# Kernel tuning notes

Measured on AMD Instinct MI355X. Metric: run time of the kernel, lower is better.

The kernel has to match this reference:

```python
import jax, jax.numpy as jnp
import numpy as np

B, S, D, H, F = 2, 4096, 768, 12, 3072
DK = D // H
EPS = 1e-5


def _layernorm(x, alpha, gamma):
    # Faithful to the custom Layernormalization: torch.std (unbiased, ddof=1),
    # (x - mean) / (std + eps), scalar alpha/gamma.
    m = jnp.mean(x, axis=-1, keepdims=True)
    s = jnp.std(x, axis=-1, ddof=1, keepdims=True)
    return alpha * ((x - m) / (s + EPS)) + gamma


def setup_inputs() -> dict:
    key = jax.random.key(0)
    ks = jax.random.split(key, 12)
    sc = 0.02
    inp = {
        "x": jax.random.normal(ks[0], (B, S, D), jnp.float32),
        # attention projections, stored as [in, out]
        "wq": jax.random.normal(ks[1], (D, D), jnp.float32) * sc,
        "bq": jnp.zeros((D,), jnp.float32),
        "wk": jax.random.normal(ks[2], (D, D), jnp.float32) * sc,
        "bk": jnp.zeros((D,), jnp.float32),
        "wv": jax.random.normal(ks[3], (D, D), jnp.float32) * sc,
        "bv": jnp.zeros((D,), jnp.float32),
        "wo": jax.random.normal(ks[4], (D, D), jnp.float32) * sc,
        "bo": jnp.zeros((D,), jnp.float32),
        # feedforward
        "w1": jax.random.normal(ks[5], (D, F), jnp.float32) * sc,
        "b1": jnp.zeros((F,), jnp.float32),
        "w2": jax.random.normal(ks[6], (F, D), jnp.float32) * sc,
        "b2": jnp.zeros((D,), jnp.float32),
        # two residual LayerNorms, scalar params (alpha=1, gamma=0 at init)
        "a1": jnp.ones((1,), jnp.float32),
        "g1": jnp.zeros((1,), jnp.float32),
        "a2": jnp.ones((1,), jnp.float32),
        "g2": jnp.zeros((1,), jnp.float32),
    }
    return inp


def reference(x, wq, bq, wk, bk, wv, bv, wo, bo, w1, b1, w2, b2, a1, g1, a2, g2):
    # --- self attention sublayer ---
    q = (x @ wq + bq).reshape(B, S, H, DK).transpose(0, 2, 1, 3)  # [B,H,S,dk]
    k = (x @ wk + bk).reshape(B, S, H, DK).transpose(0, 2, 1, 3)
    v = (x @ wv + bv).reshape(B, S, H, DK).transpose(0, 2, 1, 3)
    scores = jnp.einsum("bhqd,bhkd->bhqk", q, k) / np.sqrt(DK).astype(np.float32)
    attn = jax.nn.softmax(scores, axis=-1)  # dropout is identity (p=0 / eval)
    ctx = jnp.einsum("bhqk,bhkd->bhqd", attn, v)  # [B,H,S,dk]
    ctx = ctx.transpose(0, 2, 1, 3).reshape(B, S, D)
    attn_out = ctx @ wo + bo
    x = _layernorm(x + attn_out, a1, g1)
    # --- feedforward sublayer ---
    ff = jax.nn.relu(x @ w1 + b1) @ w2 + b2
    x = _layernorm(x + ff, a2, g2)
    return x
```

## Files before the change

### kernel.cpp

```cpp
#include <hip/hip_runtime.h>
#include <hip/hip_bf16.h>
#include <cstdint>
#include <cstddef>

typedef unsigned short u16;
typedef __attribute__((ext_vector_type(8))) __bf16 bf16x8;
typedef __attribute__((ext_vector_type(4))) float f32x4;

#define AS1 __attribute__((address_space(1)))
#define AS3 __attribute__((address_space(3)))

__device__ __forceinline__ u16 f2bf(float f) {
    union { float f; uint32_t u; } v; v.f = f;
    uint32_t r = (v.u + 0x7FFFu + ((v.u >> 16) & 1u)) >> 16;
    return (u16)r;
}

__device__ __forceinline__ float bf2f(u16 b) {
    union { uint32_t u; float f; } v; v.u = ((uint32_t)b) << 16;
    return v.f;
}

__device__ __forceinline__ uint32_t cvtpk_bf2(float lo, float hi) {
    uint32_t r;
    asm("v_cvt_pk_bf16_f32 %0, %1, %2" : "=v"(r) : "v"(lo), "v"(hi));
    return r;
}

__device__ __forceinline__ f32x4 mfma16(bf16x8 a, bf16x8 b, f32x4 c) {
    return __builtin_amdgcn_mfma_f32_16x16x32_bf16(a, b, c, 0, 0, 0);
}

__device__ __forceinline__ void async16(const u16* g, u16* lds_uniform_base) {
    __builtin_amdgcn_global_load_lds((const AS1 void*)g, (AS3 void*)lds_uniform_base, 16, 0, 0);
}

__device__ __forceinline__ int xcd_swz(int nwg) {
    int b = blockIdx.x + gridDim.x * (blockIdx.y + gridDim.y * blockIdx.z);
    return (b & 7) * (nwg >> 3) + (b >> 3);
}

__global__ __launch_bounds__(256)
void k_prep(const float* __restrict__ x, u16* __restrict__ xb,
            const float* __restrict__ wq, const float* __restrict__ wk,
            const float* __restrict__ wv, const float* __restrict__ wo,
            const float* __restrict__ w1, const float* __restrict__ w2,
            u16* __restrict__ wqkvt, u16* __restrict__ wot,
            u16* __restrict__ w1t, u16* __restrict__ w2t)
{
    int bx = blockIdx.x;
    if (bx < 6144) {
        int i = (bx * 256 + threadIdx.x) * 4;
        float4 f = *(const float4*)(x + i);
        xb[i + 0] = f2bf(f.x); xb[i + 1] = f2bf(f.y);
        xb[i + 2] = f2bf(f.z); xb[i + 3] = f2bf(f.w);
        return;
    }
    int t = bx - 6144;
    const float* in; u16* out; int R, C;
    if (t < 2304) {
        int m = t / 576; t -= m * 576;
        R = 768; C = 768;
        in = (m == 0) ? wq : (m == 1) ? wk : (m == 2) ? wv : wo;
        out = (m < 3) ? wqkvt + (size_t)m * 768 * 768 : wot;
    } else if (t < 4608) {
        t -= 2304; in = w1; out = w1t; R = 768; C = 3072;
    } else {
        t -= 4608; in = w2; out = w2t; R = 3072; C = 768;
    }
    int tilesX = C >> 5;
    int c0 = (t % tilesX) * 32, r0 = (t / tilesX) * 32;
    __shared__ float tile[32][33];
    int tx = threadIdx.x & 31, ty = threadIdx.x >> 5;
    #pragma unroll
    for (int i = ty; i < 32; i += 8)
        tile[i][tx] = in[(size_t)(r0 + i) * C + c0 + tx];
    __syncthreads();
    #pragma unroll
    for (int i = ty; i < 32; i += 8)
        out[(size_t)(c0 + i) * R + r0 + tx] = f2bf(tile[tx][i]);
}

template <bool RELU>
__global__ __launch_bounds__(256)
void k_gemm(const u16* __restrict__ A, const u16* __restrict__ Bt,
            const float* __restrict__ bias, u16* __restrict__ Cb,
            int M, int N, int K)
{
    __shared__ __align__(16) u16 lA[3 * 4096];
    __shared__ __align__(16) u16 lB[3 * 4096];
    const int tid = threadIdx.x;
    const int w = tid >> 6, lane = tid & 63;
    const int quad = lane >> 4, l15 = lane & 15;
    const int m0 = blockIdx.x * 128, n0 = blockIdx.y * 128;
    const int wm = (w >> 1) * 64, wn = (w & 1) * 64;
    const int sw = (quad ^ ((l15 >> 1) & 3)) * 8;
    const int dst = w * 512;

    const u16* pA[2]; const u16* pB[2];
    #pragma unroll
    for (int r = 0; r < 2; ++r) {
        int c = r * 256 + tid;
        int row = c >> 2, ch = (c & 3) ^ ((row >> 1) & 3);
        pA[r] = A + (size_t)(m0 + row) * K + ch * 8;
        pB[r] = Bt + (size_t)(n0 + row) * K + ch * 8;
    }

    const f32x4 fz = {0.f, 0.f, 0.f, 0.f};
    f32x4 acc[4][4];
    #pragma unroll
    for (int i = 0; i < 4; ++i)
        #pragma unroll
        for (int j = 0; j < 4; ++j) acc[i][j] = fz;

    #pragma unroll
    for (int p = 0; p < 2; ++p) {
        #pragma unroll
        for (int r = 0; r < 2; ++r) {
            async16(pA[r], lA + p * 4096 + r * 2048 + dst);
            async16(pB[r], lB + p * 4096 + r * 2048 + dst);
            pA[r] += 32; pB[r] += 32;
        }
    }

    const int nIt = K >> 5;
    int cur = 0;
    for (int it = 0; it < nIt; ++it) {
        if (it + 1 < nIt) asm volatile("s_waitcnt vmcnt(4)" ::: "memory");
        else              asm volatile("s_waitcnt vmcnt(0)" ::: "memory");
        __builtin_amdgcn_s_barrier();
        asm volatile("" ::: "memory");
        if (it + 2 < nIt) {
            int nb = cur + 2; if (nb >= 3) nb -= 3;
            #pragma unroll
            for (int r = 0; r < 2; ++r) {
                async16(pA[r], lA + nb * 4096 + r * 2048 + dst);
                async16(pB[r], lB + nb * 4096 + r * 2048 + dst);
                pA[r] += 32; pB[r] += 32;
            }
        }
        const u16* bA = lA + cur * 4096;
        const u16* bB = lB + cur * 4096;
        bf16x8 af[4], bfr[4];
        #pragma unroll
        for (int i = 0; i < 4; ++i)
            af[i] = *(const bf16x8*)&bA[(wm + i * 16 + l15) * 32 + sw];
        #pragma unroll
        for (int j = 0; j < 4; ++j)
            bfr[j] = *(const bf16x8*)&bB[(wn + j * 16 + l15) * 32 + sw];
        #pragma unroll
        for (int i = 0; i < 4; ++i)
            #pragma unroll
            for (int j = 0; j < 4; ++j)
                acc[i][j] = mfma16(af[i], bfr[j], acc[i][j]);
        asm volatile("" ::: "memory");
        cur = (cur + 1 == 3) ? 0 : cur + 1;
    }
    #pragma unroll
    for (int j = 0; j < 4; ++j) {
        int col = n0 + wn + j * 16 + l15;
        float bv = bias[col];
        #pragma unroll
        for (int i = 0; i < 4; ++i) {
            int row = m0 + wm + i * 16 + quad * 4;
            #pragma unroll
            for (int r = 0; r < 4; ++r) {
                float t = acc[i][j][r] + bv;
                if (RELU) t = fmaxf(t, 0.f);
                Cb[(size_t)(row + r) * N + col] = f2bf(t);
            }
        }
    }
}

__global__ __launch_bounds__(256)
void k_gemm_part(const u16* __restrict__ A, const u16* __restrict__ Bt,
                 float* __restrict__ C0, float* __restrict__ C1,
                 int M, int N, int K, int Kh)
{
    __shared__ __align__(16) u16 lA[3 * 4096];
    __shared__ __align__(16) u16 lB[3 * 4096];
    const int tid = threadIdx.x;
    const int w = tid >> 6, lane = tid & 63;
    const int quad = lane >> 4, l15 = lane & 15;
    const int m0 = blockIdx.x * 128, n0 = blockIdx.y * 128;
    const int wm = (w >> 1) * 64, wn = (w & 1) * 64;
    const int sw = (quad ^ ((l15 >> 1) & 3)) * 8;
    const int kbeg = blockIdx.z * Kh;
    float* __restrict__ C = blockIdx.z ? C1 : C0;
    const int dst = w * 512;

    const u16* pA[2]; const u16* pB[2];
    #pragma unroll
    for (int r = 0; r < 2; ++r) {
        int c = r * 256 + tid;
        int row = c >> 2, ch = (c & 3) ^ ((row >> 1) & 3);
        pA[r] = A + (size_t)(m0 + row) * K + kbeg + ch * 8;
        pB[r] = Bt + (size_t)(n0 + row) * K + kbeg + ch * 8;
    }

    const f32x4 fz = {0.f, 0.f, 0.f, 0.f};
    f32x4 acc[4][4];
    #pragma unroll
    for (int i = 0; i < 4; ++i)
        #pragma unroll
        for (int j = 0; j < 4; ++j) acc[i][j] = fz;

    #pragma unroll
    for (int p = 0; p < 2; ++p) {
        #pragma unroll
        for (int r = 0; r < 2; ++r) {
            async16(pA[r], lA + p * 4096 + r * 2048 + dst);
            async16(pB[r], lB + p * 4096 + r * 2048 + dst);
            pA[r] += 32; pB[r] += 32;
        }
    }

    const int nIt = Kh >> 5;
    int cur = 0;
    for (int it = 0; it < nIt; ++it) {
        if (it + 1 < nIt) asm volatile("s_waitcnt vmcnt(4)" ::: "memory");
        else              asm volatile("s_waitcnt vmcnt(0)" ::: "memory");
        __builtin_amdgcn_s_barrier();
        asm volatile("" ::: "memory");
        if (it + 2 < nIt) {
            int nb = cur + 2; if (nb >= 3) nb -= 3;
            #pragma unroll
            for (int r = 0; r < 2; ++r) {
                async16(pA[r], lA + nb * 4096 + r * 2048 + dst);
                async16(pB[r], lB + nb * 4096 + r * 2048 + dst);
                pA[r] += 32; pB[r] += 32;
            }
        }
        const u16* bA = lA + cur * 4096;
        const u16* bB = lB + cur * 4096;
        bf16x8 af[4], bfr[4];
        #pragma unroll
        for (int i = 0; i < 4; ++i)
            af[i] = *(const bf16x8*)&bA[(wm + i * 16 + l15) * 32 + sw];
        #pragma unroll
        for (int j = 0; j < 4; ++j)
            bfr[j] = *(const bf16x8*)&bB[(wn + j * 16 + l15) * 32 + sw];
        #pragma unroll
        for (int i = 0; i < 4; ++i)
            #pragma unroll
            for (int j = 0; j < 4; ++j)
                acc[i][j] = mfma16(af[i], bfr[j], acc[i][j]);
        asm volatile("" ::: "memory");
        cur = (cur + 1 == 3) ? 0 : cur + 1;
    }
    #pragma unroll
    for (int j = 0; j < 4; ++j) {
        int col = n0 + wn + j * 16 + l15;
        #pragma unroll
        for (int i = 0; i < 4; ++i) {
            int row = m0 + wm + i * 16 + quad * 4;
            #pragma unroll
            for (int r = 0; r < 4; ++r)
                C[(size_t)(row + r) * N + col] = acc[i][j][r];
        }
    }
}

__global__ __launch_bounds__(256)
void k_gemm_qkv(const u16* __restrict__ A, const u16* __restrict__ Bt,
                const float* __restrict__ bq, const float* __restrict__ bk,
                const float* __restrict__ bv,
                u16* __restrict__ qb, u16* __restrict__ kb, u16* __restrict__ vtg,
                int M, int K, float scale_q)
{
    __shared__ __align__(16) u16 qsm[24576];
    u16* lA = qsm;
    u16* lB = qsm + 12288;
    const int tid = threadIdx.x;
    const int w = tid >> 6, lane = tid & 63;
    const int quad = lane >> 4, l15 = lane & 15;
    const int m0 = blockIdx.x * 128, n0 = blockIdx.y * 128;
    const int wm = (w >> 1) * 64, wn = (w & 1) * 64;
    const int sw = (quad ^ ((l15 >> 1) & 3)) * 8;
    const int sel = blockIdx.y / 6;
    const int cl0 = n0 - sel * 768;
    const int dst = w * 512;

    const u16* pA[2]; const u16* pB[2];
    #pragma unroll
    for (int r = 0; r < 2; ++r) {
        int c = r * 256 + tid;
        int row = c >> 2, ch = (c & 3) ^ ((row >> 1) & 3);
        pA[r] = A + (size_t)(m0 + row) * K + ch * 8;
        pB[r] = Bt + (size_t)(n0 + row) * K + ch * 8;
    }

    const f32x4 fz = {0.f, 0.f, 0.f, 0.f};
    f32x4 acc[4][4];
    #pragma unroll
    for (int i = 0; i < 4; ++i)
        #pragma unroll
        for (int j = 0; j < 4; ++j) acc[i][j] = fz;

    #pragma unroll
    for (int p = 0; p < 2; ++p) {
        #pragma unroll
        for (int r = 0; r < 2; ++r) {
            async16(pA[r], lA + p * 4096 + r * 2048 + dst);
            async16(pB[r], lB + p * 4096 + r * 2048 + dst);
            pA[r] += 32; pB[r] += 32;
        }
    }

    const int nIt = K >> 5;
    int cur = 0;
    for (int it = 0; it < nIt; ++it) {
        if (it + 1 < nIt) asm volatile("s_waitcnt vmcnt(4)" ::: "memory");
        else              asm volatile("s_waitcnt vmcnt(0)" ::: "memory");
        __builtin_amdgcn_s_barrier();
        asm volatile("" ::: "memory");
        if (it + 2 < nIt) {
            int nb = cur + 2; if (nb >= 3) nb -= 3;
            #pragma unroll
            for (int r = 0; r < 2; ++r) {
                async16(pA[r], lA + nb * 4096 + r * 2048 + dst);
                async16(pB[r], lB + nb * 4096 + r * 2048 + dst);
                pA[r] += 32; pB[r] += 32;
            }
        }
        const u16* bA = lA + cur * 4096;
        const u16* bB = lB + cur * 4096;
        bf16x8 af[4], bfr[4];
        #pragma unroll
        for (int i = 0; i < 4; ++i)
            af[i] = *(const bf16x8*)&bA[(wm + i * 16 + l15) * 32 + sw];
        #pragma unroll
        for (int j = 0; j < 4; ++j)
            bfr[j] = *(const bf16x8*)&bB[(wn + j * 16 + l15) * 32 + sw];
        #pragma unroll
        for (int i = 0; i < 4; ++i)
            #pragma unroll
            for (int j = 0; j < 4; ++j)
                acc[i][j] = mfma16(af[i], bfr[j], acc[i][j]);
        asm volatile("" ::: "memory");
        cur = (cur + 1 == 3) ? 0 : cur + 1;
    }
    __syncthreads();
    const float* bias = (sel == 0) ? bq : (sel == 1) ? bk : bv;
    if (sel < 2) {
        u16* out = (sel == 0) ? qb : kb;
        float sc = (sel == 0) ? scale_q : 1.f;
        #pragma unroll
        for (int j = 0; j < 4; ++j) {
            int cl = cl0 + wn + j * 16 + l15;
            float bvv = bias[cl];
            #pragma unroll
            for (int i = 0; i < 4; ++i) {
                int row = m0 + wm + i * 16 + quad * 4;
                #pragma unroll
                for (int r = 0; r < 4; ++r)
                    out[(size_t)(row + r) * 768 + cl] = f2bf((acc[i][j][r] + bvv) * sc);
            }
        }
    } else {
        u16* lT = qsm + w * 4608;
        #pragma unroll
        for (int j = 0; j < 4; ++j) {
            float bvv = bias[cl0 + wn + j * 16 + l15];
            #pragma unroll
            for (int i = 0; i < 4; ++i)
                #pragma unroll
                for (int r = 0; r < 4; ++r)
                    lT[(j * 16 + l15) * 72 + i * 16 + quad * 4 + r]
                        = f2bf(acc[i][j][r] + bvv);
        }
        int gcol = cl0 + wn + lane;
        u16* gdst = vtg + (size_t)gcol * M + m0 + wm;
        #pragma unroll
        for (int kk = 0; kk < 8; ++kk) {
            bf16x8 v = *(const bf16x8*)&lT[lane * 72 + kk * 8];
            *(bf16x8*)(gdst + kk * 8) = v;
        }
    }
}

__global__ __launch_bounds__(256, 3)
void k_attention(const u16* __restrict__ Q, const u16* __restrict__ Kb,
                 const u16* __restrict__ Vt, u16* __restrict__ ctx,
                 int S, int D, int H, int M)
{
    __shared__ __align__(16) u16 sKV[16384];
    __shared__ float sL[2][64];
    const int o = xcd_swz(gridDim.x * gridDim.y);
    const int qt = o % gridDim.x, bh = o / gridDim.x;
    const int b = bh / H, h = bh % H;
    const int tid = threadIdx.x, w = tid >> 6, lane = tid & 63;
    const int wq = w & 1, wk = w >> 1;
    const int quad = lane >> 4, l15 = lane & 15;
    const int sw = (quad ^ ((l15 >> 1) & 3)) * 8;
    const size_t bS = (size_t)b * S;
    const int q0 = qt * 128 + wq * 64;

    bf16x8 qf[4][2];
    #pragma unroll
    for (int set = 0; set < 4; ++set)
        #pragma unroll
        for (int kc = 0; kc < 2; ++kc)
            qf[set][kc] = *(const bf16x8*)(Q + (bS + q0 + set * 16 + l15) * D
                                           + (size_t)h * 64 + kc * 32 + quad * 8);

    const f32x4 fz = {0.f, 0.f, 0.f, 0.f};
    f32x4 O[4][4], Ol[4];
    #pragma unroll
    for (int s = 0; s < 4; ++s) {
        Ol[s] = fz;
        #pragma unroll
        for (int j = 0; j < 4; ++j) O[s][j] = fz;
    }
    union { u16 s[8]; bf16x8 v; } one8;
    #pragma unroll
    for (int i = 0; i < 8; ++i) one8.s[i] = 0x3F80;

    const u16* kbase = Kb + bS * D + (size_t)h * 64;
    const u16* vbase = Vt + (size_t)h * 64 * M + bS;

    const int rsw = (lane & ~12) | ((lane & 4) << 1) | ((lane & 8) >> 1);
    const u16* gk[2]; const u16* gv[2];
    #pragma unroll
    for (int i = 0; i < 2; ++i) {
        gk[i] = kbase + (size_t)rsw * D + i * 32 + w * 8;
        int c = i * 256 + tid;
        int dk = (c >> 2) & 63, vch = (c & 3) ^ ((dk >> 1) & 3);
        gv[i] = vbase + (size_t)dk * M + i * 32 + vch * 8;
    }
    const int dslot = w * 512;

    #pragma unroll
    for (int i = 0; i < 2; ++i) {
        async16(gk[i], sKV + i * 2048 + dslot);
        async16(gv[i], sKV + 8192 + i * 2048 + dslot);
        gk[i] += (size_t)64 * D;
        gv[i] += 64;
    }

    int ksl[2];
    #pragma unroll
    for (int ks = 0; ks < 2; ++ks) {
        int row64 = wk * 32 + ((l15 >> 2) << 3) + ks * 4 + (l15 & 3);
        int s = (row64 & ~12) | ((row64 & 4) << 1) | ((row64 & 8) >> 1);
        ksl[ks] = quad * 512 + s * 8;
    }

    const int T = S >> 6;
    for (int t = 0; t < T; ++t) {
        __syncthreads();
        if (t + 1 < T) {
            int nb = (t + 1) & 1;
            #pragma unroll
            for (int i = 0; i < 2; ++i) {
                async16(gk[i], sKV + nb * 4096 + i * 2048 + dslot);
                async16(gv[i], sKV + 8192 + nb * 4096 + i * 2048 + dslot);
                gk[i] += (size_t)64 * D;
                gv[i] += 64;
            }
        }
        const u16* lKb = sKV + (t & 1) * 4096;
        const u16* lVb = sKV + 8192 + (t & 1) * 4096;

        bf16x8 ka[2][2], vf[4];
        #pragma unroll
        for (int ks = 0; ks < 2; ++ks)
            #pragma unroll
            for (int kc = 0; kc < 2; ++kc)
                ka[ks][kc] = *(const bf16x8*)&lKb[kc * 2048 + ksl[ks]];
        #pragma unroll
        for (int dj = 0; dj < 4; ++dj)
            vf[dj] = *(const bf16x8*)
                &lVb[wk * 2048 + (dj * 16 + l15) * 32 + sw];

        #pragma unroll
        for (int set = 0; set < 4; ++set) {
            f32x4 sc0 = fz, sc1 = fz;
            __builtin_amdgcn_s_setprio(1);
            sc0 = mfma16(ka[0][0], qf[set][0], sc0);
            sc0 = mfma16(ka[0][1], qf[set][1], sc0);
            sc1 = mfma16(ka[1][0], qf[set][0], sc1);
            sc1 = mfma16(ka[1][1], qf[set][1], sc1);
            __builtin_amdgcn_s_setprio(0);
            float p0[4], p1[4];
            #pragma unroll
            for (int r = 0; r < 4; ++r) {
                p0[r] = __builtin_amdgcn_exp2f(sc0[r]);
                p1[r] = __builtin_amdgcn_exp2f(sc1[r]);
            }
            union { uint32_t u[4]; bf16x8 v; } pa;
            pa.u[0] = cvtpk_bf2(p0[0], p0[1]); pa.u[1] = cvtpk_bf2(p0[2], p0[3]);
            pa.u[2] = cvtpk_bf2(p1[0], p1[1]); pa.u[3] = cvtpk_bf2(p1[2], p1[3]);
            __builtin_amdgcn_s_setprio(1);
            #pragma unroll
            for (int dj = 0; dj < 4; ++dj)
                O[set][dj] = mfma16(pa.v, vf[dj], O[set][dj]);
            Ol[set] = mfma16(pa.v, one8.v, Ol[set]);
            __builtin_amdgcn_s_setprio(0);
        }
    }

    __syncthreads();
    u16* lO = sKV;
    if (wk == 1) {
        #pragma unroll
        for (int set = 0; set < 4; ++set) {
            #pragma unroll
            for (int dj = 0; dj < 4; ++dj)
                #pragma unroll
                for (int r = 0; r < 4; ++r)
                    lO[(wq * 64 + set * 16 + quad * 4 + r) * 66 + dj * 16 + l15]
                        = f2bf(O[set][dj][r]);
            if (l15 == 0) {
                #pragma unroll
                for (int r = 0; r < 4; ++r)
                    sL[wq][set * 16 + quad * 4 + r] = Ol[set][r];
            }
        }
    }
    __syncthreads();
    if (wk == 0) {
        #pragma unroll
        for (int set = 0; set < 4; ++set) {
            float rl[4];
            #pragma unroll
            for (int r = 0; r < 4; ++r)
                rl[r] = 1.f / (Ol[set][r] + sL[wq][set * 16 + quad * 4 + r]);
            #pragma unroll
            for (int dj = 0; dj < 4; ++dj)
                #pragma unroll
                for (int r = 0; r < 4; ++r) {
                    float o = O[set][dj][r]
                        + bf2f(lO[(wq * 64 + set * 16 + quad * 4 + r) * 66 + dj * 16 + l15]);
                    ctx[(bS + q0 + set * 16 + quad * 4 + r) * D
                        + (size_t)h * 64 + dj * 16 + l15] = f2bf(o * rl[r]);
                }
        }
    }
}

__global__ __launch_bounds__(256)
void k_layernorm2(const float* __restrict__ p0, const float* __restrict__ p1,
                  const float* __restrict__ resid, const float* __restrict__ bias,
                  const float* __restrict__ a, const float* __restrict__ g,
                  float* __restrict__ outf, u16* __restrict__ outb, int D)
{
    const int row = blockIdx.x, tid = threadIdx.x;
    const size_t base = (size_t)row * D;
    float v[3];
    float s = 0.f, sq = 0.f;
    #pragma unroll
    for (int i = 0; i < 3; ++i) {
        int c = tid + i * 256;
        float x = p0[base + c] + p1[base + c] + resid[base + c] + bias[c];
        v[i] = x; s += x; sq += x * x;
    }
    #pragma unroll
    for (int off = 32; off >= 1; off >>= 1) {
        s += __shfl_xor(s, off, 64);
        sq += __shfl_xor(sq, off, 64);
    }
    __shared__ float red[8];
    const int w = tid >> 6;
    if ((tid & 63) == 0) { red[w] = s; red[4 + w] = sq; }
    __syncthreads();
    s = red[0] + red[1] + red[2] + red[3];
    sq = red[4] + red[5] + red[6] + red[7];
    float mean = s / D;
    float var = fmaxf((sq - s * mean) / (D - 1), 0.f);
    float denom = sqrtf(var) + 1e-5f;
    float av = a[0], gv = g[0];
    #pragma unroll
    for (int i = 0; i < 3; ++i) {
        float y = av * ((v[i] - mean) / denom) + gv;
        if (outf) outf[base + tid + i * 256] = y;
        if (outb) outb[base + tid + i * 256] = f2bf(y);
    }
}

extern "C" void kernel_launch(void* const* d_in, const int* in_sizes, int n_in,
                              void* d_out, int out_size, void* d_ws, size_t ws_size,
                              hipStream_t stream)
{
    constexpr int B = 2, S = 4096, D = 768, H = 12, F = 3072;
    constexpr int M = B * S;
    const float SCALE_Q = 1.4426950408889634f / 8.0f;
    const float* x  = (const float*)d_in[0];
    const float* wq = (const float*)d_in[1];
    const float* bq = (const float*)d_in[2];
    const float* wk = (const float*)d_in[3];
    const float* bk = (const float*)d_in[4];
    const float* wv = (const float*)d_in[5];
    const float* bv = (const float*)d_in[6];
    const float* wo = (const float*)d_in[7];
    const float* bo = (const float*)d_in[8];
    const float* w1 = (const float*)d_in[9];
    const float* b1 = (const float*)d_in[10];
    const float* w2 = (const float*)d_in[11];
    const float* b2 = (const float*)d_in[12];
    const float* a1 = (const float*)d_in[13];
    const float* g1 = (const float*)d_in[14];
    const float* a2 = (const float*)d_in[15];
    const float* g2 = (const float*)d_in[16];

    char* ws = (char*)d_ws;
    size_t off = 0;
    auto alloc = [&](size_t bytes) {
        void* p = ws + off;
        off = (off + bytes + 255) & ~(size_t)255;
        return p;
    };
    u16*   xb    = (u16*)alloc((size_t)M * D * 2);
    u16*   wqkvt = (u16*)alloc((size_t)3 * D * D * 2);
    u16*   wot   = (u16*)alloc((size_t)D * D * 2);
    u16*   w1t   = (u16*)alloc((size_t)D * F * 2);
    u16*   w2t   = (u16*)alloc((size_t)D * F * 2);
    u16*   qb    = (u16*)alloc((size_t)M * D * 2);
    u16*   kb    = (u16*)alloc((size_t)M * D * 2);
    u16*   vtg   = (u16*)alloc((size_t)M * D * 2);
    u16*   ctxb  = (u16*)alloc((size_t)M * D * 2);
    float* x1f   = (float*)alloc((size_t)M * D * 4);
    u16*   x1b   = (u16*)alloc((size_t)M * D * 2);
    u16*   ff1b  = (u16*)alloc((size_t)M * F * 2);

    float* p0a = (float*)qb;
    float* p1a = (float*)ff1b;
    float* p0b = (float*)qb;
    float* p1b = (float*)vtg;

    k_prep<<<6144 + 6912, 256, 0, stream>>>(x, xb, wq, wk, wv, wo, w1, w2,
                                            wqkvt, wot, w1t, w2t);

    k_gemm_qkv<<<dim3(M / 128, 3 * D / 128), 256, 0, stream>>>(
        xb, wqkvt, bq, bk, bv, qb, kb, vtg, M, D, SCALE_Q);

    k_attention<<<dim3(S / 128, B * H), 256, 0, stream>>>(qb, kb, vtg, ctxb, S, D, H, M);

    k_gemm_part<<<dim3(M / 128, D / 128, 2), 256, 0, stream>>>(
        ctxb, wot, p0a, p1a, M, D, D, D / 2);
    k_layernorm2<<<M, 256, 0, stream>>>(p0a, p1a, x, bo, a1, g1, x1f, x1b, D);

    k_gemm<true><<<dim3(M / 128, F / 128), 256, 0, stream>>>(
        x1b, w1t, b1, ff1b, M, F, D);
    k_gemm_part<<<dim3(M / 128, D / 128, 2), 256, 0, stream>>>(
        ff1b, w2t, p0b, p1b, M, D, F, F / 2);
    k_layernorm2<<<M, 256, 0, stream>>>(p0b, p1b, x1f, b2, a2, g2, (float*)d_out, nullptr, D);

    (void)in_sizes; (void)n_in; (void)out_size; (void)ws_size;
}
```

Before: 418.8 us.

## Enlarge GEMM block tiles to 256x128 with 512 threads and double buffering

The plain and split-K GEMM kernels now run 8 waves per block on a 256x128 output tile instead of 4 waves on 128x128. This halves the B-tile reloads per output row and shrinks the grid. The three-stage async LDS pipeline with explicit vmcnt waits is replaced by a two-stage double buffer synchronised with __syncthreads. That is simpler, but it overlaps loads less and waits for every outstanding load each iteration. The smaller grid also risks underfilling the CUs for the output-projection and FFN2 kernels.

Result: slower. 428.7 us (+2.4%).

```diff
diff --git a/kernel.cpp b/kernel.cpp
--- a/kernel.cpp
+++ b/kernel.cpp
@@ -82,28 +82,31 @@
 }
 
 template <bool RELU>
-__global__ __launch_bounds__(256)
+__global__ __launch_bounds__(512)
 void k_gemm(const u16* __restrict__ A, const u16* __restrict__ Bt,
             const float* __restrict__ bias, u16* __restrict__ Cb,
             int M, int N, int K)
 {
-    __shared__ __align__(16) u16 lA[3 * 4096];
-    __shared__ __align__(16) u16 lB[3 * 4096];
+    __shared__ __align__(16) u16 lA[2 * 8192];
+    __shared__ __align__(16) u16 lB[2 * 4096];
     const int tid = threadIdx.x;
     const int w = tid >> 6, lane = tid & 63;
     const int quad = lane >> 4, l15 = lane & 15;
-    const int m0 = blockIdx.x * 128, n0 = blockIdx.y * 128;
+    const int m0 = blockIdx.x * 256, n0 = blockIdx.y * 128;
     const int wm = (w >> 1) * 64, wn = (w & 1) * 64;
     const int sw = (quad ^ ((l15 >> 1) & 3)) * 8;
-    const int dst = w * 512;
-
-    const u16* pA[2]; const u16* pB[2];
+
+    const u16* pA[2]; const u16* pB;
     #pragma unroll
     for (int r = 0; r < 2; ++r) {
-        int c = r * 256 + tid;
+        int c = r * 512 + tid;
         int row = c >> 2, ch = (c & 3) ^ ((row >> 1) & 3);
         pA[r] = A + (size_t)(m0 + row) * K + ch * 8;
-        pB[r] = Bt + (size_t)(n0 + row) * K + ch * 8;
+    }
+    {
+        int c = tid;
+        int row = c >> 2, ch = (c & 3) ^ ((row >> 1) & 3);
+        pB = Bt + (size_t)(n0 + row) * K + ch * 8;
     }
 
     const f32x4 fz = {0.f, 0.f, 0.f, 0.f};
@@ -114,33 +117,28 @@
         for (int j = 0; j < 4; ++j) acc[i][j] = fz;
 
     #pragma unroll
-    for (int p = 0; p < 2; ++p) {
-        #pragma unroll
-        for (int r = 0; r < 2; ++r) {
-            async16(pA[r], lA + p * 4096 + r * 2048 + dst);
-            async16(pB[r], lB + p * 4096 + r * 2048 + dst);
-            pA[r] += 32; pB[r] += 32;
-        }
-    }
+    for (int r = 0; r < 2; ++r) {
+        async16(pA[r], lA + r * 4096 + w * 512);
+        pA[r] += 32;
+    }
+    async16(pB, lB + w * 512);
+    pB += 32;
 
     const int nIt = K >> 5;
-    int cur = 0;
     for (int it = 0; it < nIt; ++it) {
-        if (it + 1 < nIt) asm volatile("s_waitcnt vmcnt(4)" ::: "memory");
-        else              asm volatile("s_waitcnt vmcnt(0)" ::: "memory");
-        __builtin_amdgcn_s_barrier();
-        asm volatile("" ::: "memory");
-        if (it + 2 < nIt) {
-            int nb = cur + 2; if (nb >= 3) nb -= 3;
+        __syncthreads();
+        if (it + 1 < nIt) {
+            int nb = (it + 1) & 1;
             #pragma unroll
             for (int r = 0; r < 2; ++r) {
-                async16(pA[r], lA + nb * 4096 + r * 2048 + dst);
-                async16(pB[r], lB + nb * 4096 + r * 2048 + dst);
-                pA[r] += 32; pB[r] += 32;
-            }
-        }
-        const u16* bA = lA + cur * 4096;
-        const u16* bB = lB + cur * 4096;
+                async16(pA[r], lA + nb * 8192 + r * 4096 + w * 512);
+                pA[r] += 32;
+            }
+            async16(pB, lB + nb * 4096 + w * 512);
+            pB += 32;
+        }
+        const u16* bA = lA + (it & 1) * 8192;
+        const u16* bB = lB + (it & 1) * 4096;
         bf16x8 af[4], bfr[4];
         #pragma unroll
         for (int i = 0; i < 4; ++i)
@@ -153,8 +151,6 @@
             #pragma unroll
             for (int j = 0; j < 4; ++j)
                 acc[i][j] = mfma16(af[i], bfr[j], acc[i][j]);
-        asm volatile("" ::: "memory");
-        cur = (cur + 1 == 3) ? 0 : cur + 1;
     }
     #pragma unroll
     for (int j = 0; j < 4; ++j) {
@@ -173,30 +169,33 @@
     }
 }
 
-__global__ __launch_bounds__(256)
+__global__ __launch_bounds__(512)
 void k_gemm_part(const u16* __restrict__ A, const u16* __restrict__ Bt,
                  float* __restrict__ C0, float* __restrict__ C1,
                  int M, int N, int K, int Kh)
 {
-    __shared__ __align__(16) u16 lA[3 * 4096];
-    __shared__ __align__(16) u16 lB[3 * 4096];
+    __shared__ __align__(16) u16 lA[2 * 8192];
+    __shared__ __align__(16) u16 lB[2 * 4096];
     const int tid = threadIdx.x;
     const int w = tid >> 6, lane = tid & 63;
     const int quad = lane >> 4, l15 = lane & 15;
-    const int m0 = blockIdx.x * 128, n0 = blockIdx.y * 128;
+    const int m0 = blockIdx.x * 256, n0 = blockIdx.y * 128;
     const int wm = (w >> 1) * 64, wn = (w & 1) * 64;
     const int sw = (quad ^ ((l15 >> 1) & 3)) * 8;
     const int kbeg = blockIdx.z * Kh;
     float* __restrict__ C = blockIdx.z ? C1 : C0;
-    const int dst = w * 512;
-
-    const u16* pA[2]; const u16* pB[2];
+
+    const u16* pA[2]; const u16* pB;
     #pragma unroll
     for (int r = 0; r < 2; ++r) {
-        int c = r * 256 + tid;
+        int c = r * 512 + tid;
         int row = c >> 2, ch = (c & 3) ^ ((row >> 1) & 3);
         pA[r] = A + (size_t)(m0 + row) * K + kbeg + ch * 8;
-        pB[r] = Bt + (size_t)(n0 + row) * K + kbeg + ch * 8;
+    }
+    {
+        int c = tid;
+        int row = c >> 2, ch = (c & 3) ^ ((row >> 1) & 3);
+        pB = Bt + (size_t)(n0 + row) * K + kbeg + ch * 8;
     }
 
     const f32x4 fz = {0.f, 0.f, 0.f, 0.f};
@@ -207,33 +206,28 @@
         for (int j = 0; j < 4; ++j) acc[i][j] = fz;
 
     #pragma unroll
-    for (int p = 0; p < 2; ++p) {
-        #pragma unroll
-        for (int r = 0; r < 2; ++r) {
-            async16(pA[r], lA + p * 4096 + r * 2048 + dst);
-            async16(pB[r], lB + p * 4096 + r * 2048 + dst);
-            pA[r] += 32; pB[r] += 32;
-        }
-    }
+    for (int r = 0; r < 2; ++r) {
+        async16(pA[r], lA + r * 4096 + w * 512);
+        pA[r] += 32;
+    }
+    async16(pB, lB + w * 512);
+    pB += 32;
 
     const int nIt = Kh >> 5;
-    int cur = 0;
     for (int it = 0; it < nIt; ++it) {
-        if (it + 1 < nIt) asm volatile("s_waitcnt vmcnt(4)" ::: "memory");
-        else              asm volatile("s_waitcnt vmcnt(0)" ::: "memory");
-        __builtin_amdgcn_s_barrier();
-        asm volatile("" ::: "memory");
-        if (it + 2 < nIt) {
-            int nb = cur + 2; if (nb >= 3) nb -= 3;
+        __syncthreads();
+        if (it + 1 < nIt) {
+            int nb = (it + 1) & 1;
             #pragma unroll
             for (int r = 0; r < 2; ++r) {
-                async16(pA[r], lA + nb * 4096 + r * 2048 + dst);
-                async16(pB[r], lB + nb * 4096 + r * 2048 + dst);
-                pA[r] += 32; pB[r] += 32;
-            }
-        }
-        const u16* bA = lA + cur * 4096;
-        const u16* bB = lB + cur * 4096;
+                async16(pA[r], lA + nb * 8192 + r * 4096 + w * 512);
+                pA[r] += 32;
+            }
+            async16(pB, lB + nb * 4096 + w * 512);
+            pB += 32;
+        }
+        const u16* bA = lA + (it & 1) * 8192;
+        const u16* bB = lB + (it & 1) * 4096;
         bf16x8 af[4], bfr[4];
         #pragma unroll
         for (int i = 0; i < 4; ++i)
@@ -246,8 +240,6 @@
             #pragma unroll
             for (int j = 0; j < 4; ++j)
                 acc[i][j] = mfma16(af[i], bfr[j], acc[i][j]);
-        asm volatile("" ::: "memory");
-        cur = (cur + 1 == 3) ? 0 : cur + 1;
     }
     #pragma unroll
     for (int j = 0; j < 4; ++j) {
@@ -637,13 +629,13 @@
 
     k_attention<<<dim3(S / 128, B * H), 256, 0, stream>>>(qb, kb, vtg, ctxb, S, D, H, M);
 
-    k_gemm_part<<<dim3(M / 128, D / 128, 2), 256, 0, stream>>>(
+    k_gemm_part<<<dim3(M / 256, D / 128, 2), 512, 0, stream>>>(
         ctxb, wot, p0a, p1a, M, D, D, D / 2);
     k_layernorm2<<<M, 256, 0, stream>>>(p0a, p1a, x, bo, a1, g1, x1f, x1b, D);
 
-    k_gemm<true><<<dim3(M / 128, F / 128), 256, 0, stream>>>(
+    k_gemm<true><<<dim3(M / 256, F / 128), 512, 0, stream>>>(
         x1b, w1t, b1, ff1b, M, F, D);
-    k_gemm_part<<<dim3(M / 128, D / 128, 2), 256, 0, stream>>>(
+    k_gemm_part<<<dim3(M / 256, D / 128, 2), 512, 0, stream>>>(
         ff1b, w2t, p0b, p1b, M, D, F, F / 2);
     k_layernorm2<<<M, 256, 0, stream>>>(p0b, p1b, x1f, b2, a2, g2, (float*)d_out, nullptr, D);
 
```
